# Kernel tuning notes

Measured on AMD Instinct MI355X. Metric: run time of the kernel, lower is better.

## Reference

```python
import jax, jax.numpy as jnp
import numpy as np

B, C, H, W = 16, 512, 64, 64
L, D = 77, 768
NH = 8
HD = C // NH
EPS = 1e-5


def layernorm(x, g, b):
    m = jnp.mean(x, axis=-1, keepdims=True)
    v = jnp.var(x, axis=-1, keepdims=True)
    return (x - m) * jax.lax.rsqrt(v + EPS) * g + b


def setup_inputs() -> dict:
    key = jax.random.key(0)
    ks = jax.random.split(key, 12)
    s_c = 1.0 / np.sqrt(C)
    s_d = 1.0 / np.sqrt(D)
    return {
        "x": jax.random.normal(ks[0], (B, C, H, W), jnp.float32),
        "text_features": jax.random.normal(ks[1], (B, L, D), jnp.float32),
        "wq": jax.random.normal(ks[2], (C, C), jnp.float32) * s_c,
        "bq": jnp.zeros((C,), jnp.float32),
        "wk": jax.random.normal(ks[3], (C, D), jnp.float32) * s_d,
        "bk": jnp.zeros((C,), jnp.float32),
        "wv": jax.random.normal(ks[4], (C, D), jnp.float32) * s_d,
        "bv": jnp.zeros((C,), jnp.float32),
        "wo": jax.random.normal(ks[5], (C, C), jnp.float32) * s_c,
        "bo": jnp.zeros((C,), jnp.float32),
        "g1": jnp.ones((C,), jnp.float32),
        "b1": jnp.zeros((C,), jnp.float32),
        "g2": jnp.ones((C,), jnp.float32),
        "b2": jnp.zeros((C,), jnp.float32),
    }


def reference(x, text_features, wq, bq, wk, bk, wv, bv, wo, bo, g1, b1, g2, b2):
    b, c, h, w = x.shape
    # 1x1 conv query projection
    q = jnp.einsum('bchw,oc->bohw', x, wq) + bq[None, :, None, None]
    # 2D positional encoding: first c/2 channels vary along w, next c/2 along h
    pos_x = jnp.broadcast_to(jnp.linspace(0.0, 1.0, w)[None, :], (h, w))
    pos_y = jnp.broadcast_to(jnp.linspace(0.0, 1.0, h)[:, None], (h, w))
    pe = jnp.concatenate([
        jnp.broadcast_to(pos_x[None], (c // 2, h, w)),
        jnp.broadcast_to(pos_y[None], (c // 2, h, w)),
    ], axis=0)  # [C,H,W]
    q = q + 0.05 * pe[None]
    # flatten spatial -> tokens, layernorm over channels
    q_flat = q.reshape(b, c, h * w).transpose(0, 2, 1)  # [B,HW,C]
    q_norm = layernorm(q_flat, g1, b1)
    qh = q_norm.reshape(b, h * w, NH, HD)  # [B,HW,NH,HD]
    # text key/value projections
    k = jnp.einsum('bld,cd->blc', text_features, wk) + bk
    v = jnp.einsum('bld,cd->blc', text_features, wv) + bv
    k_norm = layernorm(k, g2, b2)
    kh = k_norm.reshape(b, -1, NH, HD)
    vh = v.reshape(b, -1, NH, HD)
    scale = HD ** -0.5
    attn = jnp.einsum('bqhd,bkhd->bhqk', qh, kh) * scale  # [B,NH,HW,L]
    attn = jax.nn.softmax(attn, axis=-1)  # dropout is identity in eval
    out = jnp.einsum('bhqk,bkhd->bqhd', attn, vh).reshape(b, h * w, c)
    out = out.transpose(0, 2, 1).reshape(b, c, h, w)
    out = jnp.einsum('bchw,oc->bohw', out, wo) + bo[None, :, None, None]
    return out + x
```

## Files before the change

### kernel.cpp

```cpp
#include <hip/hip_runtime.h>
#include <stdint.h>

#define BD   16
#define CD   512
#define HD_  64
#define NH_  8
#define HWD  4096
#define LD   77
#define DD   768

typedef __bf16 bf16;
typedef bf16 bf16x8 __attribute__((ext_vector_type(8)));
typedef float f32x4 __attribute__((ext_vector_type(4)));

__device__ __forceinline__ void async16(const bf16* g, bf16* l) {
  __builtin_amdgcn_global_load_lds(
      (const __attribute__((address_space(1))) void*)g,
      (__attribute__((address_space(3))) void*)l, 16, 0, 0);
}

__device__ __forceinline__ unsigned short bfb(float f) {
  bf16 h = (bf16)f;
  return __builtin_bit_cast(unsigned short, h);
}

__global__ __launch_bounds__(256) void xpose_cvt(const float* __restrict__ X,
                                                 bf16* __restrict__ Y) {
  __shared__ float tile[64][68];
  const int b = blockIdx.z, c0 = blockIdx.y * 64, t0 = blockIdx.x * 64;
  const int tid = threadIdx.x;
  const float* Xb = X + ((size_t)b * CD + c0) * HWD + t0;
#pragma unroll
  for (int p = 0; p < 4; ++p) {
    int c = (tid >> 4) + p * 16;
    int t = (tid & 15) * 4;
    float4 v = *(const float4*)(Xb + (size_t)c * HWD + t);
    *(float4*)&tile[c][t] = v;
  }
  __syncthreads();
  int t = tid >> 2, cb = (tid & 3) * 16;
  union { uint4 u[2]; unsigned short us[16]; } pk;
#pragma unroll
  for (int j = 0; j < 16; ++j) pk.us[j] = bfb(tile[cb + j][t]);
  uint4* Yp = (uint4*)(Y + ((size_t)(b * HWD + t0 + t)) * CD + c0 + cb);
  Yp[0] = pk.u[0];
  Yp[1] = pk.u[1];
}

__global__ void cvt_bf16_k(const float* __restrict__ X, bf16* __restrict__ Y, int n) {
  int i = (blockIdx.x * 256 + threadIdx.x) * 8;
  if (i >= n) return;
  float4 a = *(const float4*)(X + i);
  float4 c = *(const float4*)(X + i + 4);
  union { uint4 u; unsigned short us[8]; } pk;
  pk.us[0] = bfb(a.x); pk.us[1] = bfb(a.y); pk.us[2] = bfb(a.z); pk.us[3] = bfb(a.w);
  pk.us[4] = bfb(c.x); pk.us[5] = bfb(c.y); pk.us[6] = bfb(c.z); pk.us[7] = bfb(c.w);
  *(uint4*)(Y + i) = pk.u;
}

template <int TM, int TN, int MODE>
__global__ __launch_bounds__(256)
void gemm_bt(const bf16* __restrict__ A, const bf16* __restrict__ B,
             int M, int N, int K,
             const float* __restrict__ bias, const float* __restrict__ xres,
             float* __restrict__ D) {
  constexpr int WM = TM / 2, WN = TN / 2;
  constexpr int AFR = WM / 16, BFR = WN / 16;
  constexpr int ACH = TM / 8, TCH = (TM + TN) / 8, WCH = TCH / 4;
  __shared__ bf16 sA[TM * 64];
  __shared__ bf16 sB[TN * 64];
  const int tid = threadIdx.x, wave = tid >> 6, lane = tid & 63;
  const int m0 = blockIdx.y * TM, n0 = blockIdx.x * TN;
  const int wm = (wave >> 1) * WM, wn = (wave & 1) * WN;
  const int sub = lane >> 3, col8 = (lane & 7) * 8;
  const int mlo = lane & 15, khi = lane >> 4;
  f32x4 acc[AFR][BFR] = {};

  for (int k0 = 0; k0 < K; k0 += 64) {
#pragma unroll
    for (int r = 0; r < WCH; ++r) {
      int ci = wave * WCH + r;
      if (ci < ACH) {
        int row = ci * 8 + sub;
        int g = m0 + row;
        if (g > M - 1) g = M - 1;
        async16(A + (size_t)g * K + k0 + col8, &sA[ci * 512]);
      } else {
        int cj = ci - ACH;
        int row = cj * 8 + sub;
        async16(B + (size_t)(n0 + row) * K + k0 + col8, &sB[cj * 512]);
      }
    }
    __syncthreads();
#pragma unroll
    for (int kc = 0; kc < 2; ++kc) {
      bf16x8 af[AFR], bfv[BFR];
      const int ko = kc * 32 + khi * 8;
#pragma unroll
      for (int i = 0; i < AFR; ++i)
        af[i] = *(const bf16x8*)&sA[(wm + i * 16 + mlo) * 64 + ko];
#pragma unroll
      for (int j = 0; j < BFR; ++j)
        bfv[j] = *(const bf16x8*)&sB[(wn + j * 16 + mlo) * 64 + ko];
#pragma unroll
      for (int i = 0; i < AFR; ++i)
#pragma unroll
        for (int j = 0; j < BFR; ++j)
          acc[i][j] = __builtin_amdgcn_mfma_f32_16x16x32_bf16(af[i], bfv[j],
                                                              acc[i][j], 0, 0, 0);
    }
    __syncthreads();
  }

#pragma unroll
  for (int i = 0; i < AFR; ++i) {
    const int mb = m0 + wm + i * 16 + khi * 4;
#pragma unroll
    for (int j = 0; j < BFR; ++j) {
      const int n = n0 + wn + j * 16 + mlo;
#pragma unroll
      for (int r = 0; r < 4; ++r) {
        const int m = mb + r;
        float val = acc[i][j][r];
        if constexpr (MODE == 0) {
          int hw = m & (HWD - 1);
          float pe = (n < 256) ? (float)(hw & 63) : (float)(hw >> 6);
          val += bias[n] + (0.05f / 63.0f) * pe;
          D[(size_t)m * CD + n] = val;
        } else if constexpr (MODE == 1) {
          if (m < M) D[(size_t)m * CD + n] = val + bias[n];
        } else {
          int b = n >> 12, hw = n & (HWD - 1);
          size_t addr = ((size_t)(b * CD + m)) * HWD + hw;
          D[addr] = val + bias[m] + xres[addr];
        }
      }
    }
  }
}

__global__ __launch_bounds__(256) void ln_rows(const float* __restrict__ X,
                                               const float* __restrict__ gg,
                                               const float* __restrict__ bb,
                                               bf16* __restrict__ Y, int nrows,
                                               int khlayout) {
  const int wv = threadIdx.x >> 6, lane = threadIdx.x & 63;
  const int row = blockIdx.x * 4 + wv;
  if (row >= nrows) return;
  const float* xr = X + (size_t)row * CD + lane * 8;
  float4 v0 = *(const float4*)xr;
  float4 v1 = *(const float4*)(xr + 4);
  float xv[8] = {v0.x, v0.y, v0.z, v0.w, v1.x, v1.y, v1.z, v1.w};
  float s = 0.f, sq = 0.f;
#pragma unroll
  for (int j = 0; j < 8; ++j) { s += xv[j]; sq += xv[j] * xv[j]; }
#pragma unroll
  for (int off = 1; off < 64; off <<= 1) {
    s += __shfl_xor(s, off);
    sq += __shfl_xor(sq, off);
  }
  float mean = s * (1.0f / 512.0f);
  float var = sq * (1.0f / 512.0f) - mean * mean;
  float rstd = rsqrtf(var + 1e-5f);
  const int c0 = lane * 8;
  union { uint4 u; unsigned short us[8]; } pk;
#pragma unroll
  for (int j = 0; j < 8; ++j)
    pk.us[j] = bfb((xv[j] - mean) * rstd * gg[c0 + j] + bb[c0 + j]);
  size_t ya;
  if (khlayout) {
    int bq = row / LD, l = row - bq * LD;
    int hh = lane >> 3, dd = (lane & 7) * 8;
    ya = (((size_t)(bq * NH_ + hh)) * LD + l) * HD_ + dd;
  } else {
    ya = (size_t)row * CD + c0;
  }
  *(uint4*)(Y + ya) = pk.u;
}

__global__ __launch_bounds__(256) void make_vt(const float* __restrict__ vraw,
                                               bf16* __restrict__ vt) {
  const int bh = blockIdx.x, b = bh >> 3, h = bh & 7;
  const int tid = threadIdx.x, d = tid & 63, lg = tid >> 6;
  for (int l = lg; l < 96; l += 4) {
    float v = 0.f;
    if (l < LD) v = vraw[((size_t)(b * LD + l)) * CD + h * HD_ + d];
    vt[((size_t)(bh * HD_ + d)) * 96 + l] = (bf16)v;
  }
}

__global__ __launch_bounds__(256) void attn_k(const bf16* __restrict__ Q,
                                              const bf16* __restrict__ KH,
                                              const bf16* __restrict__ VT,
                                              bf16* __restrict__ O) {
  __shared__ bf16 P[4][16 * 104];
  const int tid = threadIdx.x, wv = tid >> 6, lane = tid & 63;
  const int m = lane & 15, kg = lane >> 4;
  const int q0 = blockIdx.x * 64, h = blockIdx.y, b = blockIdx.z;
  const int bh = b * NH_ + h;

  const size_t qoff = ((size_t)(b * HWD + q0 + wv * 16 + m)) * CD + h * HD_;
  bf16x8 a0 = *(const bf16x8*)(Q + qoff + kg * 8);
  bf16x8 a1 = *(const bf16x8*)(Q + qoff + 32 + kg * 8);

  const bf16* Kb = KH + (size_t)bh * LD * HD_;
  f32x4 s[5];
#pragma unroll
  for (int kt = 0; kt < 5; ++kt) {
    int key = kt * 16 + m;
    if (key > LD - 1) key = LD - 1;
    const bf16* kr = Kb + key * HD_ + kg * 8;
    bf16x8 b0 = *(const bf16x8*)kr;
    bf16x8 b1 = *(const bf16x8*)(kr + 32);
    f32x4 z = {0.f, 0.f, 0.f, 0.f};
    z = __builtin_amdgcn_mfma_f32_16x16x32_bf16(a0, b0, z, 0, 0, 0);
    z = __builtin_amdgcn_mfma_f32_16x16x32_bf16(a1, b1, z, 0, 0, 0);
    s[kt] = z;
  }

  bf16* Pw = &P[wv][0];
#pragma unroll
  for (int r = 0; r < 4; ++r) {
    float sc[5];
#pragma unroll
    for (int kt = 0; kt < 5; ++kt) {
      float v = s[kt][r] * 0.125f;
      if (kt == 4 && m >= LD - 64) v = -3.0e38f;
      sc[kt] = v;
    }
    float mx = fmaxf(fmaxf(fmaxf(sc[0], sc[1]), fmaxf(sc[2], sc[3])), sc[4]);
    mx = fmaxf(mx, __shfl_xor(mx, 1));
    mx = fmaxf(mx, __shfl_xor(mx, 2));
    mx = fmaxf(mx, __shfl_xor(mx, 4));
    mx = fmaxf(mx, __shfl_xor(mx, 8));
    float sum = 0.f;
#pragma unroll
    for (int kt = 0; kt < 5; ++kt) {
      sc[kt] = __expf(sc[kt] - mx);
      sum += sc[kt];
    }
    sum += __shfl_xor(sum, 1);
    sum += __shfl_xor(sum, 2);
    sum += __shfl_xor(sum, 4);
    sum += __shfl_xor(sum, 8);
    float inv = 1.0f / sum;
    const int prow = kg * 4 + r;
#pragma unroll
    for (int kt = 0; kt < 5; ++kt)
      Pw[prow * 104 + kt * 16 + m] = (bf16)(sc[kt] * inv);
    Pw[prow * 104 + 80 + m] = (bf16)0.f;
  }
  __syncthreads();

  bf16x8 ap[3];
#pragma unroll
  for (int kc = 0; kc < 3; ++kc)
    ap[kc] = *(const bf16x8*)&Pw[m * 104 + kc * 32 + kg * 8];

  const bf16* Vb = VT + (size_t)bh * HD_ * 96;
  f32x4 o[4] = {};
#pragma unroll
  for (int nt = 0; nt < 4; ++nt) {
#pragma unroll
    for (int kc = 0; kc < 3; ++kc) {
      bf16x8 bv = *(const bf16x8*)(Vb + (nt * 16 + m) * 96 + kc * 32 + kg * 8);
      o[nt] = __builtin_amdgcn_mfma_f32_16x16x32_bf16(ap[kc], bv, o[nt], 0, 0, 0);
    }
  }
#pragma unroll
  for (int nt = 0; nt < 4; ++nt)
#pragma unroll
    for (int r = 0; r < 4; ++r) {
      const int row = b * HWD + q0 + wv * 16 + kg * 4 + r;
      O[(size_t)row * CD + h * HD_ + nt * 16 + m] = (bf16)(o[nt][r]);
    }
}

extern "C" void kernel_launch(void* const* d_in, const int* in_sizes, int n_in,
                              void* d_out, int out_size, void* d_ws, size_t ws_size,
                              hipStream_t stream) {
  const float* x    = (const float*)d_in[0];
  const float* text = (const float*)d_in[1];
  const float* wq   = (const float*)d_in[2];
  const float* bq   = (const float*)d_in[3];
  const float* wk   = (const float*)d_in[4];
  const float* bk   = (const float*)d_in[5];
  const float* wv   = (const float*)d_in[6];
  const float* bv   = (const float*)d_in[7];
  const float* wo   = (const float*)d_in[8];
  const float* bo   = (const float*)d_in[9];
  const float* g1   = (const float*)d_in[10];
  const float* b1   = (const float*)d_in[11];
  const float* g2   = (const float*)d_in[12];
  const float* b2   = (const float*)d_in[13];
  float* out = (float*)d_out;

  char* p = (char*)d_ws;
  auto alloc = [&](size_t bytes) {
    char* r = p;
    p += (bytes + 255) & ~(size_t)255;
    return r;
  };
  bf16* xt     = (bf16*)alloc((size_t)BD * HWD * CD * 2);
  bf16* attn_o = (bf16*)alloc((size_t)BD * HWD * CD * 2);
  bf16* textb  = (bf16*)alloc((size_t)BD * LD * DD * 2);
  bf16* wqb    = (bf16*)alloc((size_t)CD * CD * 2);
  bf16* wkb    = (bf16*)alloc((size_t)CD * DD * 2);
  bf16* wvb    = (bf16*)alloc((size_t)CD * DD * 2);
  bf16* wob    = (bf16*)alloc((size_t)CD * CD * 2);
  float* kraw  = (float*)alloc((size_t)BD * LD * CD * 4);
  float* vraw  = (float*)alloc((size_t)BD * LD * CD * 4);
  bf16* kh     = (bf16*)alloc((size_t)BD * NH_ * LD * HD_ * 2);
  bf16* vt     = (bf16*)alloc((size_t)BD * NH_ * HD_ * 96 * 2);
  float* qraw = out;
  bf16* qbf = xt;

  xpose_cvt<<<dim3(HWD / 64, CD / 64, BD), 256, 0, stream>>>(x, xt);
  const int nt_ = BD * LD * DD;
  cvt_bf16_k<<<(nt_ / 8 + 255) / 256, 256, 0, stream>>>(text, textb, nt_);
  cvt_bf16_k<<<(CD * CD / 8 + 255) / 256, 256, 0, stream>>>(wq, wqb, CD * CD);
  cvt_bf16_k<<<(CD * DD / 8 + 255) / 256, 256, 0, stream>>>(wk, wkb, CD * DD);
  cvt_bf16_k<<<(CD * DD / 8 + 255) / 256, 256, 0, stream>>>(wv, wvb, CD * DD);
  cvt_bf16_k<<<(CD * CD / 8 + 255) / 256, 256, 0, stream>>>(wo, wob, CD * CD);

  gemm_bt<128, 128, 1><<<dim3(4, 10), 256, 0, stream>>>(
      textb, wkb, BD * LD, CD, DD, bk, nullptr, kraw);
  gemm_bt<128, 128, 1><<<dim3(4, 10), 256, 0, stream>>>(
      textb, wvb, BD * LD, CD, DD, bv, nullptr, vraw);
  ln_rows<<<(BD * LD) / 4, 256, 0, stream>>>(kraw, g2, b2, kh, BD * LD, 1);
  make_vt<<<BD * NH_, 256, 0, stream>>>(vraw, vt);

  gemm_bt<128, 256, 0><<<dim3(2, 512), 256, 0, stream>>>(
      xt, wqb, BD * HWD, CD, CD, bq, nullptr, qraw);
  ln_rows<<<(BD * HWD) / 4, 256, 0, stream>>>(qraw, g1, b1, qbf, BD * HWD, 0);

  attn_k<<<dim3(HWD / 64, NH_, BD), 256, 0, stream>>>(qbf, kh, vt, attn_o);

  gemm_bt<256, 128, 3><<<dim3(512, 2), 256, 0, stream>>>(
      wob, attn_o, CD, BD * HWD, CD, bo, x, out);
}
```

Before: 628.8 us.

## Fuse query projection GEMM with positional encoding and LayerNorm

Replaces the Q-projection GEMM, which wrote fp32 output, and the separate LayerNorm pass with one kernel. Each block computes a full 64-row by 512-column tile, adds bias and positional encoding, reduces row statistics through shuffles and shared memory, and writes normalized bf16 directly. This removes the fp32 intermediate write and reread (about 128MB each way) and one launch. In exchange the tile shape is changed, so the whole 512-wide weight slice is reloaded per block without double buffering, and occupancy may drop.

```diff
diff --git a/kernel.cpp b/kernel.cpp
--- a/kernel.cpp
+++ b/kernel.cpp
@@ -122,12 +122,7 @@
       for (int r = 0; r < 4; ++r) {
         const int m = mb + r;
         float val = acc[i][j][r];
-        if constexpr (MODE == 0) {
-          int hw = m & (HWD - 1);
-          float pe = (n < 256) ? (float)(hw & 63) : (float)(hw >> 6);
-          val += bias[n] + (0.05f / 63.0f) * pe;
-          D[(size_t)m * CD + n] = val;
-        } else if constexpr (MODE == 1) {
+        if constexpr (MODE == 1) {
           if (m < M) D[(size_t)m * CD + n] = val + bias[n];
         } else {
           int b = n >> 12, hw = n & (HWD - 1);
@@ -135,6 +130,115 @@
           D[addr] = val + bias[m] + xres[addr];
         }
       }
+    }
+  }
+}
+
+__global__ __launch_bounds__(256) void qgemm_ln(const bf16* __restrict__ A,
+                                                const bf16* __restrict__ Bw,
+                                                const float* __restrict__ bias,
+                                                const float* __restrict__ g1,
+                                                const float* __restrict__ b1,
+                                                bf16* __restrict__ Y) {
+  constexpr int TM = 64, KK = 512;
+  constexpr int AFR = 4, BFR = 8;
+  __shared__ bf16 sA[TM * 64];
+  __shared__ bf16 sB[512 * 64];
+  __shared__ float sStat[4][TM][2];
+  const int tid = threadIdx.x, wave = tid >> 6, lane = tid & 63;
+  const int m0 = blockIdx.x * TM;
+  const int wn = wave * 128;
+  const int sub = lane >> 3, col8 = (lane & 7) * 8;
+  const int mlo = lane & 15, khi = lane >> 4;
+  f32x4 acc[AFR][BFR] = {};
+
+  for (int k0 = 0; k0 < KK; k0 += 64) {
+#pragma unroll
+    for (int r = 0; r < 18; ++r) {
+      int ci = wave * 18 + r;
+      if (ci < 8) {
+        int row = ci * 8 + sub;
+        async16(A + (size_t)(m0 + row) * KK + k0 + col8, &sA[ci * 512]);
+      } else {
+        int cj = ci - 8;
+        int row = cj * 8 + sub;
+        async16(Bw + (size_t)row * KK + k0 + col8, &sB[cj * 512]);
+      }
+    }
+    __syncthreads();
+#pragma unroll
+    for (int kc = 0; kc < 2; ++kc) {
+      const int ko = kc * 32 + khi * 8;
+      bf16x8 af[AFR], bfv[BFR];
+#pragma unroll
+      for (int i = 0; i < AFR; ++i)
+        af[i] = *(const bf16x8*)&sA[(i * 16 + mlo) * 64 + ko];
+#pragma unroll
+      for (int j = 0; j < BFR; ++j)
+        bfv[j] = *(const bf16x8*)&sB[(wn + j * 16 + mlo) * 64 + ko];
+#pragma unroll
+      for (int i = 0; i < AFR; ++i)
+#pragma unroll
+        for (int j = 0; j < BFR; ++j)
+          acc[i][j] = __builtin_amdgcn_mfma_f32_16x16x32_bf16(af[i], bfv[j],
+                                                              acc[i][j], 0, 0, 0);
+    }
+    __syncthreads();
+  }
+
+  float cb[8], cg[8], ct[8];
+#pragma unroll
+  for (int j = 0; j < 8; ++j) {
+    int n = wn + j * 16 + mlo;
+    cb[j] = bias[n];
+    cg[j] = g1[n];
+    ct[j] = b1[n];
+  }
+
+#pragma unroll
+  for (int i = 0; i < AFR; ++i) {
+#pragma unroll
+    for (int r = 0; r < 4; ++r) {
+      const int row = i * 16 + khi * 4 + r;
+      const int hw = (m0 + row) & (HWD - 1);
+      const float pex = (float)(hw & 63) * (0.05f / 63.0f);
+      const float pey = (float)(hw >> 6) * (0.05f / 63.0f);
+      float s = 0.f, sq = 0.f;
+#pragma unroll
+      for (int j = 0; j < 8; ++j) {
+        float v = acc[i][j][r] + cb[j] + ((wn + j * 16) < 256 ? pex : pey);
+        acc[i][j][r] = v;
+        s += v;
+        sq += v * v;
+      }
+      s += __shfl_xor(s, 1);  sq += __shfl_xor(sq, 1);
+      s += __shfl_xor(s, 2);  sq += __shfl_xor(sq, 2);
+      s += __shfl_xor(s, 4);  sq += __shfl_xor(sq, 4);
+      s += __shfl_xor(s, 8);  sq += __shfl_xor(sq, 8);
+      if (mlo == 0) {
+        sStat[wave][row][0] = s;
+        sStat[wave][row][1] = sq;
+      }
+    }
+  }
+  __syncthreads();
+
+#pragma unroll
+  for (int i = 0; i < AFR; ++i) {
+#pragma unroll
+    for (int r = 0; r < 4; ++r) {
+      const int row = i * 16 + khi * 4 + r;
+      float s = sStat[0][row][0] + sStat[1][row][0] +
+                sStat[2][row][0] + sStat[3][row][0];
+      float sq = sStat[0][row][1] + sStat[1][row][1] +
+                 sStat[2][row][1] + sStat[3][row][1];
+      float mean = s * (1.0f / 512.0f);
+      float var = sq * (1.0f / 512.0f) - mean * mean;
+      float rstd = rsqrtf(var + 1e-5f);
+      bf16* yr = Y + (size_t)(m0 + row) * CD + wn + mlo;
+#pragma unroll
+      for (int j = 0; j < 8; ++j)
+        yr[j * 16] = (bf16)((acc[i][j][r] - mean) * rstd * cg[j] + ct[j]);
     }
   }
 }
@@ -312,8 +416,7 @@
   float* vraw  = (float*)alloc((size_t)BD * LD * CD * 4);
   bf16* kh     = (bf16*)alloc((size_t)BD * NH_ * LD * HD_ * 2);
   bf16* vt     = (bf16*)alloc((size_t)BD * NH_ * HD_ * 96 * 2);
-  float* qraw = out;
-  bf16* qbf = xt;
+  bf16* qbf = (bf16*)out;
 
   xpose_cvt<<<dim3(HWD / 64, CD / 64, BD), 256, 0, stream>>>(x, xt);
   const int nt_ = BD * LD * DD;
@@ -327,12 +430,10 @@
       textb, wkb, BD * LD, CD, DD, bk, nullptr, kraw);
   gemm_bt<128, 128, 1><<<dim3(4, 10), 256, 0, stream>>>(
       textb, wvb, BD * LD, CD, DD, bv, nullptr, vraw);
-  ln_rows<<<(BD * LD) / 4, 256, 0, stream>>>(kraw, g2, b2, kh, BD * LD, 1);
+  ln_rows<<<(BD * LD + 3) / 4, 256, 0, stream>>>(kraw, g2, b2, kh, BD * LD, 1);
   make_vt<<<BD * NH_, 256, 0, stream>>>(vraw, vt);
 
-  gemm_bt<128, 256, 0><<<dim3(2, 512), 256, 0, stream>>>(
-      xt, wqb, BD * HWD, CD, CD, bq, nullptr, qraw);
-  ln_rows<<<(BD * HWD) / 4, 256, 0, stream>>>(qraw, g1, b1, qbf, BD * HWD, 0);
+  qgemm_ln<<<dim3(BD * HWD / 64), 256, 0, stream>>>(xt, wqb, bq, g1, b1, qbf);
 
   attn_k<<<dim3(HWD / 64, NH_, BD), 256, 0, stream>>>(qbf, kh, vt, attn_o);
 
```

New measurement: 611.1 us. -2.8%, faster.
